# Performance work log

Measured on AMD Instinct MI355X. Metric: run time of the kernel, lower is better.

Reference implementation:

```python
import jax, jax.numpy as jnp
import numpy as np

N_HEADS = 16


def _rotate_half(x):
    x_even = x[..., ::2]
    x_odd = x[..., 1::2]
    return jnp.stack((-x_odd, x_even), axis=-1).reshape(x.shape)


def _apply_rope(x, cos, sin):
    # cos/sin: (S, d_head) broadcast against (B, H, S, d_head)
    return x * cos + _rotate_half(x) * sin


def setup_inputs() -> dict:
    key = jax.random.key(0)
    k1, k2, k3 = jax.random.split(key, 3)
    B, S, D, H = 2, 2048, 1024, N_HEADS
    dh = D // H
    x = jax.random.normal(k1, (B, S, D), dtype=jnp.float32)
    w_qkv = jax.random.normal(k2, (D, 3 * D), dtype=jnp.float32) * 0.02
    w_proj = jax.random.normal(k3, (D, D), dtype=jnp.float32) * 0.02
    # standard interleaved RoPE tables, shape (S, d_head)
    inv_freq = 1.0 / (10000.0 ** (jnp.arange(0, dh, 2, dtype=jnp.float32) / dh))
    angles = jnp.arange(S, dtype=jnp.float32)[:, None] * inv_freq[None, :]  # (S, dh/2)
    rope_cos = jnp.repeat(jnp.cos(angles), 2, axis=-1)  # (S, dh)
    rope_sin = jnp.repeat(jnp.sin(angles), 2, axis=-1)
    return {"x": x, "w_qkv": w_qkv, "w_proj": w_proj, "rope_cos": rope_cos, "rope_sin": rope_sin}


def reference(x, w_qkv, w_proj, rope_cos, rope_sin):
    B, S, D = x.shape
    H = N_HEADS
    dh = D // H
    half = dh // 2
    qkv = x @ w_qkv  # (B, S, 3D)
    q, k, v = jnp.split(qkv, 3, axis=-1)
    # (B, S, D) -> (B, H, S, dh)
    q = q.reshape(B, S, H, dh).transpose(0, 2, 1, 3)
    k = k.reshape(B, S, H, dh).transpose(0, 2, 1, 3)
    v = v.reshape(B, S, H, dh).transpose(0, 2, 1, 3)
    q = _apply_rope(q, rope_cos, rope_sin)
    k = _apply_rope(k, rope_cos, rope_sin)
    scale = half ** -0.5
    # dual score matrices from the two half-subspaces
    attn_up = jnp.einsum('bhid,bhjd->bhij', q[..., :half], k[..., :half]) * scale
    attn_down = jnp.einsum('bhid,bhjd->bhij', q[..., half:], k[..., half:]) * scale
    lower_mask = jnp.tril(jnp.ones((S, S), dtype=bool))  # j <= i -> down
    attn_logits = jnp.where(lower_mask, attn_down, attn_up)
    attn_weights = jax.nn.softmax(attn_logits, axis=-1)
    attn_out = jnp.einsum('bhij,bhjd->bhid', attn_weights, v)
    attn_out = attn_out.transpose(0, 2, 1, 3).reshape(B, S, D)
    return attn_out @ w_proj
```

## Files before the change

kernel.cpp:

```cpp
#include <hip/hip_runtime.h>
#include <hip/hip_bf16.h>
#include <stdint.h>

typedef __bf16 bf16;
typedef __attribute__((ext_vector_type(4))) __bf16 bf16x4;
typedef __attribute__((ext_vector_type(8))) __bf16 bf16x8;
typedef __attribute__((ext_vector_type(4))) float f32x4;

#define MFMA16(a, b, c) __builtin_amdgcn_mfma_f32_16x16x32_bf16((a), (b), (c), 0, 0, 0)

#define QSC (0.17677669529663687f * 1.4426950408889634f)

__device__ __forceinline__ void async_cp16(const bf16* g, bf16* l) {
  __builtin_amdgcn_global_load_lds(
      (const __attribute__((address_space(1))) void*)g,
      (__attribute__((address_space(3))) void*)l, 16, 0, 0);
}

__global__ __launch_bounds__(256) void prep_k(const float* __restrict__ x,
                                              bf16* __restrict__ xb,
                                              const float* __restrict__ wqkv,
                                              bf16* __restrict__ wqkvT,
                                              const float* __restrict__ wproj,
                                              bf16* __restrict__ wprojT) {
  __shared__ bf16 t[64][65];
  const int bid = blockIdx.x;
  if (bid < 1024) {
    int i = (bid * 256 + threadIdx.x) * 4;
    const int stride = 1024 * 256 * 4;
    for (; i < 4194304; i += stride) {
      const f32x4 f = *(const f32x4*)(x + i);
      bf16x4 o;
      o[0] = (bf16)f[0]; o[1] = (bf16)f[1]; o[2] = (bf16)f[2]; o[3] = (bf16)f[3];
      *(bf16x4*)(xb + i) = o;
    }
    return;
  }
  const float* in;
  bf16* out;
  int R, C, tb;
  if (bid < 1792) { in = wqkv; out = wqkvT; R = 1024; C = 3072; tb = bid - 1024; }
  else            { in = wproj; out = wprojT; R = 1024; C = 1024; tb = bid - 1792; }
  const int tilesx = C >> 6;
  const int bc = (tb % tilesx) * 64, br = (tb / tilesx) * 64;
  const int tx = threadIdx.x & 63, ty = threadIdx.x >> 6;
#pragma unroll
  for (int r = ty; r < 64; r += 4) t[r][tx] = (bf16)in[(br + r) * C + bc + tx];
  __syncthreads();
#pragma unroll
  for (int r = ty; r < 64; r += 4) out[(bc + r) * R + br + tx] = t[tx][r];
}

template <int MODE, int BM>
__global__ __launch_bounds__(256) void gemm128(
    const bf16* __restrict__ A, const bf16* __restrict__ BT, int M, int N, int K,
    float* __restrict__ C, bf16* __restrict__ qws, bf16* __restrict__ kws,
    bf16* __restrict__ vT, const float* __restrict__ ropeC, const float* __restrict__ ropeS) {
  constexpr int MT = BM / 32;
  __shared__ __align__(16) bf16 As[BM * 64];
  __shared__ __align__(16) bf16 Bs[128 * 64];
  const int tid = threadIdx.x;
  const int lane = tid & 63, wave = tid >> 6;
  const int l16 = lane & 15, quad = lane >> 4;
  const int wm = (wave >> 1) * (BM / 2), wn = (wave & 1) * 64;
  const int bm = blockIdx.y, bn = blockIdx.x;

  const int srow = tid >> 3;
  const int schunk = ((tid & 7) - srow) & 7;
  const bf16* ag = A + (bm * BM + srow) * K + schunk * 8;
  const bf16* bg = BT + (bn * 128 + srow) * K + schunk * 8;
  bf16* la = &As[tid * 8];
  bf16* lb = &Bs[tid * 8];

  f32x4 acc[MT][4] = {};

  for (int k0 = 0; k0 < K; k0 += 64) {
    async_cp16(ag + k0, la);
    async_cp16(ag + 32 * K + k0, la + 2048);
    if (BM == 128) {
      async_cp16(ag + 64 * K + k0, la + 4096);
      async_cp16(ag + 96 * K + k0, la + 6144);
    }
    async_cp16(bg + k0, lb);
    async_cp16(bg + 32 * K + k0, lb + 2048);
    async_cp16(bg + 64 * K + k0, lb + 4096);
    async_cp16(bg + 96 * K + k0, lb + 6144);
    __syncthreads();
#pragma unroll
    for (int ks = 0; ks < 2; ++ks) {
      bf16x8 af[MT], bff[4];
#pragma unroll
      for (int t = 0; t < MT; ++t) {
        const int r = wm + t * 16 + l16;
        af[t] = *(const bf16x8*)&As[r * 64 + ((ks * 4 + quad + r) & 7) * 8];
      }
#pragma unroll
      for (int t = 0; t < 4; ++t) {
        const int r = wn + t * 16 + l16;
        bff[t] = *(const bf16x8*)&Bs[r * 64 + ((ks * 4 + quad + r) & 7) * 8];
      }
#pragma unroll
      for (int mt = 0; mt < MT; ++mt)
#pragma unroll
        for (int nt = 0; nt < 4; ++nt) acc[mt][nt] = MFMA16(af[mt], bff[nt], acc[mt][nt]);
    }
    __syncthreads();
  }

  if (MODE == 0) {
#pragma unroll
    for (int mt = 0; mt < MT; ++mt)
#pragma unroll
      for (int i = 0; i < 4; ++i) {
        const int row = bm * BM + wm + mt * 16 + quad * 4 + i;
#pragma unroll
        for (int nt = 0; nt < 4; ++nt) {
          const int col = bn * 128 + wn + nt * 16 + l16;
          C[row * N + col] = acc[mt][nt][i];
        }
      }
  } else {
    bf16* tb = &Bs[wave * 512];
#pragma unroll
    for (int mt = 0; mt < MT; ++mt) {
      const int s0 = bm * BM + wm + mt * 16;
      const int b = s0 >> 11, sbase = s0 & 2047;
#pragma unroll
      for (int nt = 0; nt < 4; ++nt) {
        const int colb = bn * 128 + wn + nt * 16;
        const int sec = colb >> 10, rem = colb & 1023;
        const int h = rem >> 6, d0 = rem & 63;
        if (sec < 2) {
          const int d = d0 + l16;
#pragma unroll
          for (int i = 0; i < 4; ++i) {
            const int s = sbase + quad * 4 + i;
            float v = acc[mt][nt][i];
            float pr = __shfl_xor(v, 1);
            float rot = (d & 1) ? pr : -pr;
            float rv = v * ropeC[s * 64 + d] + rot * ropeS[s * 64 + d];
            if (sec == 0) rv *= QSC;
            tb[(quad * 4 + i) * 20 + l16] = (bf16)rv;
          }
          bf16* dst = ((sec == 0) ? qws : kws) + ((b * 16 + h) * 2048 + sbase) * 64 + d0;
          bf16x4 seg = *(const bf16x4*)&tb[l16 * 20 + quad * 4];
          *(bf16x4*)(dst + l16 * 64 + quad * 4) = seg;
        } else {
          const int d = d0 + l16;
          const int s4 = sbase + quad * 4;
          const int a = (s4 >> 4) & 3;
          const int p = (s4 & ~63) | ((a >> 1) * 32 + quad * 8 + (a & 1) * 4);
          bf16x4 pk;
#pragma unroll
          for (int i = 0; i < 4; ++i) pk[i] = (bf16)acc[mt][nt][i];
          *(bf16x4*)(vT + ((b * 16 + h) * 64 + d) * 2048 + p) = pk;
        }
      }
    }
  }
}

__global__ __launch_bounds__(256) void attn_k(const bf16* __restrict__ qws,
                                              const bf16* __restrict__ kws,
                                              const bf16* __restrict__ vT,
                                              bf16* __restrict__ aw) {
  __shared__ __align__(16) bf16 Ks[2][64 * 64];
  __shared__ __align__(16) bf16 Vs[2][64 * 64];
  const int tid = threadIdx.x;
  const int lane = tid & 63, wave = tid >> 6;
  const int l16 = lane & 15, quad = lane >> 4;
  const int bh = blockIdx.x >> 4, qblk = blockIdx.x & 15;
  const int b = bh >> 4, h = bh & 15;
  const int rbase = qblk * 128 + wave * 32;

  const bf16* qb = qws + (bh * 2048 + rbase) * 64;
  const bf16* kb = kws + bh * 2048 * 64;
  const bf16* vb = vT + bh * 64 * 2048;

  const int r0 = wave * 16 + (lane >> 3);
  const int c0 = ((lane & 7) - r0) & 7;
  const bf16* kst0 = kb + r0 * 64 + c0 * 8;
  const bf16* kst1 = kb + (r0 + 8) * 64 + c0 * 8;
  const bf16* vst0 = vb + r0 * 2048 + c0 * 8;
  const bf16* vst1 = vb + (r0 + 8) * 2048 + c0 * 8;

#define STAGE(jtv)                                         \
  {                                                        \
    bf16* kdst = &Ks[(jtv) & 1][wave * 1024];              \
    bf16* vdst = &Vs[(jtv) & 1][wave * 1024];              \
    async_cp16(kst0 + (jtv) * 4096, kdst);                 \
    async_cp16(kst1 + (jtv) * 4096, kdst + 512);           \
    async_cp16(vst0 + (jtv) * 64, vdst);                   \
    async_cp16(vst1 + (jtv) * 64, vdst + 512);             \
  }

  bf16x8 qf[2][2];
#pragma unroll
  for (int g = 0; g < 2; ++g)
#pragma unroll
    for (int hf = 0; hf < 2; ++hf)
      qf[g][hf] = *(const bf16x8*)(qb + (g * 16 + l16) * 64 + hf * 32 + quad * 8);

  bf16x8 ones;
#pragma unroll
  for (int j = 0; j < 8; ++j) ones[j] = (bf16)1.0f;

  f32x4 o[2][4] = {};
  f32x4 o_l[2] = {};
  const f32x4 zz = {};
  const int tdw = rbase >> 6;

#define ATTN_BODY(TM, jt)                                                             \
  {                                                                                   \
    const bf16* Kb = Ks[(jt) & 1];                                                    \
    const bf16* Vb = Vs[(jt) & 1];                                                    \
    bf16x8 vf[2][4];                                                                  \
    _Pragma("unroll") for (int ks = 0; ks < 2; ++ks)                                  \
      _Pragma("unroll") for (int ntd = 0; ntd < 4; ++ntd)                             \
        vf[ks][ntd] = *(const bf16x8*)(Vb + (ntd * 16 + l16) * 64 +                   \
                                       ((ks * 4 + quad + l16) & 7) * 8);              \
    bf16x8 kfU[2][2], kfD[2][2];                                                      \
    _Pragma("unroll") for (int ks = 0; ks < 2; ++ks)                                  \
      _Pragma("unroll") for (int s = 0; s < 2; ++s) {                                 \
        const int ro = ((ks * 2 + s) * 16 + l16) * 64;                                \
        if (TM != 0) kfU[ks][s] = *(const bf16x8*)(Kb + ro + ((quad + l16) & 7) * 8); \
        if (TM != 2)                                                                  \
          kfD[ks][s] = *(const bf16x8*)(Kb + ro + ((4 + quad + l16) & 7) * 8);        \
      }                                                                               \
    if ((jt) + 1 < 32) STAGE((jt) + 1)                                                \
    _Pragma("unroll") for (int ks = 0; ks < 2; ++ks) {                                \
      f32x4 sU[2][2], sD[2][2];                                                       \
      _Pragma("unroll") for (int s = 0; s < 2; ++s)                                   \
        _Pragma("unroll") for (int g = 0; g < 2; ++g) {                               \
          if (TM != 0) sU[s][g] = MFMA16(kfU[ks][s], qf[g][0], zz);                   \
          if (TM != 2) sD[s][g] = MFMA16(kfD[ks][s], qf[g][1], zz);                   \
        }                                                                             \
      _Pragma("unroll") for (int g = 0; g < 2; ++g) {                                 \
        bf16x8 af;                                                                    \
        _Pragma("unroll") for (int s = 0; s < 2; ++s)                                 \
          _Pragma("unroll") for (int r = 0; r < 4; ++r) {                             \
            float x;                                                                  \
            if (TM == 0) x = sD[s][g][r];                                             \
            else if (TM == 2) x = sU[s][g][r];                                        \
            else {                                                                    \
              const int jcol = (jt) * 64 + (ks * 2 + s) * 16 + quad * 4 + r;          \
              x = (jcol <= rbase + g * 16 + l16) ? sD[s][g][r] : sU[s][g][r];         \
            }                                                                         \
            af[s * 4 + r] = (bf16)__builtin_amdgcn_exp2f(x);                          \
          }                                                                           \
        o_l[g] = MFMA16(af, ones, o_l[g]);                                            \
        _Pragma("unroll") for (int ntd = 0; ntd < 4; ++ntd)                           \
            o[g][ntd] = MFMA16(af, vf[ks][ntd], o[g][ntd]);                           \
      }                                                                               \
    }                                                                                 \
  }

  STAGE(0)
  for (int jt = 0; jt < 32; ++jt) {
    asm volatile("s_waitcnt vmcnt(0)" ::: "memory");
    __syncthreads();
    if (jt < tdw) ATTN_BODY(0, jt)
    else if (jt == tdw) ATTN_BODY(1, jt)
    else ATTN_BODY(2, jt)
  }
#undef ATTN_BODY
#undef STAGE

#pragma unroll
  for (int g = 0; g < 2; ++g) {
    float ir[4];
#pragma unroll
    for (int r = 0; r < 4; ++r) ir[r] = __builtin_amdgcn_rcpf(o_l[g][r]);
#pragma unroll
    for (int ntd = 0; ntd < 4; ++ntd)
#pragma unroll
      for (int r = 0; r < 4; ++r)
        aw[(b * 2048 + rbase + g * 16 + quad * 4 + r) * 1024 + h * 64 + ntd * 16 + l16] =
            (bf16)(o[g][ntd][r] * ir[r]);
  }
}

extern "C" void kernel_launch(void* const* d_in, const int* in_sizes, int n_in,
                              void* d_out, int out_size, void* d_ws, size_t ws_size,
                              hipStream_t stream) {
  const float* x = (const float*)d_in[0];
  const float* w_qkv = (const float*)d_in[1];
  const float* w_proj = (const float*)d_in[2];
  const float* ropeC = (const float*)d_in[3];
  const float* ropeS = (const float*)d_in[4];
  float* out = (float*)d_out;

  char* ws = (char*)d_ws;
  bf16* xb = (bf16*)ws;     ws += (size_t)4194304 * 2;
  bf16* wqkvT = (bf16*)ws;  ws += (size_t)3145728 * 2;
  bf16* wprojT = (bf16*)ws; ws += (size_t)1048576 * 2;
  bf16* qws = (bf16*)ws;    ws += (size_t)4194304 * 2;
  bf16* kws = (bf16*)ws;    ws += (size_t)4194304 * 2;
  bf16* vT = (bf16*)ws;     ws += (size_t)4194304 * 2;
  bf16* aw = (bf16*)ws;     ws += (size_t)4194304 * 2;

  prep_k<<<2048, 256, 0, stream>>>(x, xb, w_qkv, wqkvT, w_proj, wprojT);
  gemm128<1, 128><<<dim3(3072 / 128, 4096 / 128), 256, 0, stream>>>(
      xb, wqkvT, 4096, 3072, 1024, nullptr, qws, kws, vT, ropeC, ropeS);
  attn_k<<<512, 256, 0, stream>>>(qws, kws, vT, aw);
  gemm128<0, 64><<<dim3(1024 / 128, 4096 / 64), 256, 0, stream>>>(
      aw, wprojT, 4096, 1024, 1024, out, nullptr, nullptr, nullptr, nullptr, nullptr);
}
```

Baseline: 185.0 us.

## Split attention over two key halves with a merge kernel

```diff
diff --git a/kernel.cpp b/kernel.cpp
--- a/kernel.cpp
+++ b/kernel.cpp
@@ -160,18 +160,32 @@
   }
 }
 
+template <int SPLIT>
 __global__ __launch_bounds__(256) void attn_k(const bf16* __restrict__ qws,
                                               const bf16* __restrict__ kws,
                                               const bf16* __restrict__ vT,
-                                              bf16* __restrict__ aw) {
+                                              bf16* __restrict__ awA, bf16* __restrict__ pB,
+                                              float* __restrict__ lA, float* __restrict__ lB) {
   __shared__ __align__(16) bf16 Ks[2][64 * 64];
   __shared__ __align__(16) bf16 Vs[2][64 * 64];
   const int tid = threadIdx.x;
   const int lane = tid & 63, wave = tid >> 6;
   const int l16 = lane & 15, quad = lane >> 4;
-  const int bh = blockIdx.x >> 4, qblk = blockIdx.x & 15;
+  int bh, qblk, kh;
+  if (SPLIT) {
+    bh = blockIdx.x & 31;
+    const int q2 = blockIdx.x >> 5;
+    qblk = q2 >> 1;
+    kh = q2 & 1;
+  } else {
+    bh = blockIdx.x >> 4;
+    qblk = blockIdx.x & 15;
+    kh = 0;
+  }
   const int b = bh >> 4, h = bh & 15;
   const int rbase = qblk * 128 + wave * 32;
+  const int jt0 = kh * 16;
+  const int jt1 = SPLIT ? jt0 + 16 : 32;
 
   const bf16* qb = qws + (bh * 2048 + rbase) * 64;
   const bf16* kb = kws + bh * 2048 * 64;
@@ -227,7 +241,7 @@
         if (TM != 2)                                                                  \
           kfD[ks][s] = *(const bf16x8*)(Kb + ro + ((4 + quad + l16) & 7) * 8);        \
       }                                                                               \
-    if ((jt) + 1 < 32) STAGE((jt) + 1)                                                \
+    if ((jt) + 1 < jt1) STAGE((jt) + 1)                                               \
     _Pragma("unroll") for (int ks = 0; ks < 2; ++ks) {                                \
       f32x4 sU[2][2], sD[2][2];                                                       \
       _Pragma("unroll") for (int s = 0; s < 2; ++s)                                   \
@@ -255,8 +269,8 @@
     }                                                                                 \
   }
 
-  STAGE(0)
-  for (int jt = 0; jt < 32; ++jt) {
+  STAGE(jt0)
+  for (int jt = jt0; jt < jt1; ++jt) {
     asm volatile("s_waitcnt vmcnt(0)" ::: "memory");
     __syncthreads();
     if (jt < tdw) ATTN_BODY(0, jt)
@@ -266,18 +280,56 @@
 #undef ATTN_BODY
 #undef STAGE
 
-#pragma unroll
-  for (int g = 0; g < 2; ++g) {
-    float ir[4];
-#pragma unroll
-    for (int r = 0; r < 4; ++r) ir[r] = __builtin_amdgcn_rcpf(o_l[g][r]);
-#pragma unroll
-    for (int ntd = 0; ntd < 4; ++ntd)
-#pragma unroll
-      for (int r = 0; r < 4; ++r)
-        aw[(b * 2048 + rbase + g * 16 + quad * 4 + r) * 1024 + h * 64 + ntd * 16 + l16] =
-            (bf16)(o[g][ntd][r] * ir[r]);
-  }
+  if (SPLIT) {
+    bf16* p = kh ? pB : awA;
+    float* lp = kh ? lB : lA;
+#pragma unroll
+    for (int g = 0; g < 2; ++g) {
+#pragma unroll
+      for (int ntd = 0; ntd < 4; ++ntd)
+#pragma unroll
+        for (int r = 0; r < 4; ++r)
+          p[(b * 2048 + rbase + g * 16 + quad * 4 + r) * 1024 + h * 64 + ntd * 16 + l16] =
+              (bf16)o[g][ntd][r];
+      if (l16 == 0)
+#pragma unroll
+        for (int r = 0; r < 4; ++r)
+          lp[bh * 2048 + rbase + g * 16 + quad * 4 + r] = o_l[g][r];
+    }
+  } else {
+#pragma unroll
+    for (int g = 0; g < 2; ++g) {
+      float ir[4];
+#pragma unroll
+      for (int r = 0; r < 4; ++r) ir[r] = __builtin_amdgcn_rcpf(o_l[g][r]);
+#pragma unroll
+      for (int ntd = 0; ntd < 4; ++ntd)
+#pragma unroll
+        for (int r = 0; r < 4; ++r)
+          awA[(b * 2048 + rbase + g * 16 + quad * 4 + r) * 1024 + h * 64 + ntd * 16 + l16] =
+              (bf16)(o[g][ntd][r] * ir[r]);
+    }
+  }
+}
+
+__global__ __launch_bounds__(256) void merge_k(const bf16* __restrict__ pA,
+                                               const bf16* __restrict__ pB,
+                                               const float* __restrict__ lA,
+                                               const float* __restrict__ lB,
+                                               bf16* __restrict__ aw) {
+  const int i = (blockIdx.x * 256 + threadIdx.x) * 4;
+  const int rowg = i >> 10;
+  const int col = i & 1023;
+  const int b = rowg >> 11, s = rowg & 2047, h = col >> 6;
+  const int bh = b * 16 + h;
+  const float l = lA[bh * 2048 + s] + lB[bh * 2048 + s];
+  const float ir = __builtin_amdgcn_rcpf(l);
+  const bf16x4 a = *(const bf16x4*)(pA + i);
+  const bf16x4 bb = *(const bf16x4*)(pB + i);
+  bf16x4 o;
+#pragma unroll
+  for (int j = 0; j < 4; ++j) o[j] = (bf16)(((float)a[j] + (float)bb[j]) * ir);
+  *(bf16x4*)(aw + i) = o;
 }
 
 extern "C" void kernel_launch(void* const* d_in, const int* in_sizes, int n_in,
@@ -298,11 +350,22 @@
   bf16* kws = (bf16*)ws;    ws += (size_t)4194304 * 2;
   bf16* vT = (bf16*)ws;     ws += (size_t)4194304 * 2;
   bf16* aw = (bf16*)ws;     ws += (size_t)4194304 * 2;
+  bf16* pA = (bf16*)ws;     ws += (size_t)4194304 * 2;
+  bf16* pB = (bf16*)ws;     ws += (size_t)4194304 * 2;
+  float* lA = (float*)ws;   ws += (size_t)65536 * 4;
+  float* lB = (float*)ws;   ws += (size_t)65536 * 4;
+  const size_t need_split = (size_t)(ws - (char*)d_ws);
+  const bool use_split = ws_size >= need_split;
 
   prep_k<<<2048, 256, 0, stream>>>(x, xb, w_qkv, wqkvT, w_proj, wprojT);
   gemm128<1, 128><<<dim3(3072 / 128, 4096 / 128), 256, 0, stream>>>(
       xb, wqkvT, 4096, 3072, 1024, nullptr, qws, kws, vT, ropeC, ropeS);
-  attn_k<<<512, 256, 0, stream>>>(qws, kws, vT, aw);
+  if (use_split) {
+    attn_k<1><<<1024, 256, 0, stream>>>(qws, kws, vT, pA, pB, lA, lB);
+    merge_k<<<4096, 256, 0, stream>>>(pA, pB, lA, lB, aw);
+  } else {
+    attn_k<0><<<512, 256, 0, stream>>>(qws, kws, vT, aw, nullptr, nullptr, nullptr);
+  }
   gemm128<0, 64><<<dim3(1024 / 128, 4096 / 64), 256, 0, stream>>>(
       aw, wprojT, 4096, 1024, 1024, out, nullptr, nullptr, nullptr, nullptr, nullptr);
 }
```

Result: no change. 185.2 us (+0.1%).
